# Optimization experiments

Hardware: AMD Instinct MI355X
Metric: run time of the kernel (lower is better)

Reference implementation:

```python
import jax, jax.numpy as jnp
import numpy as np

N, E, DIN, HID, HEADS = 50000, 400000, 256, 64, 4
EPS_BN = 1e-5

def setup_inputs() -> dict:
    key = jax.random.key(0)
    ks = jax.random.split(key, 12)
    inp = {}
    inp['x'] = jax.random.normal(ks[0], (N, DIN), dtype=jnp.float32)
    inp['edge_index'] = jax.random.randint(ks[1], (2, E), 0, N, dtype=jnp.int64)
    s = 1.0 / np.sqrt(DIN)
    inp['W1'] = jax.random.uniform(ks[2], (DIN, HEADS * HID), jnp.float32, -s, s)
    inp['a_src1'] = jax.random.normal(ks[3], (HEADS, HID), dtype=jnp.float32) * 0.1
    inp['a_dst1'] = jax.random.normal(ks[4], (HEADS, HID), dtype=jnp.float32) * 0.1
    inp['b1'] = jnp.zeros((HEADS * HID,), jnp.float32)
    inp['bn1_w'] = jnp.ones((HEADS * HID,), jnp.float32)
    inp['bn1_b'] = jnp.zeros((HEADS * HID,), jnp.float32)
    inp['bn1_m'] = jnp.zeros((HEADS * HID,), jnp.float32)
    inp['bn1_v'] = jnp.ones((HEADS * HID,), jnp.float32)
    s2 = 1.0 / np.sqrt(HEADS * HID)
    inp['W2'] = jax.random.uniform(ks[5], (HEADS * HID, HID), jnp.float32, -s2, s2)
    inp['a_src2'] = jax.random.normal(ks[6], (1, HID), dtype=jnp.float32) * 0.1
    inp['a_dst2'] = jax.random.normal(ks[7], (1, HID), dtype=jnp.float32) * 0.1
    inp['b2'] = jnp.zeros((HID,), jnp.float32)
    inp['bn2_w'] = jnp.ones((HID,), jnp.float32)
    inp['bn2_b'] = jnp.zeros((HID,), jnp.float32)
    inp['bn2_m'] = jnp.zeros((HID,), jnp.float32)
    inp['bn2_v'] = jnp.ones((HID,), jnp.float32)
    sr = 1.0 / np.sqrt(HID)
    inp['Wr'] = jax.random.uniform(ks[8], (HID, 1), jnp.float32, -sr, sr)
    inp['br'] = jnp.zeros((1,), jnp.float32)
    inp['Wc'] = jax.random.uniform(ks[9], (HID, 1), jnp.float32, -sr, sr)
    inp['bc'] = jnp.zeros((1,), jnp.float32)
    return inp

def gat_layer(x, src, dst, W, a_src, a_dst, bias, concat):
    # x: [N, Fin] -> h: [N, H, D]
    H, D = a_src.shape
    h = (x @ W).reshape(-1, H, D)
    alpha_s = jnp.sum(h * a_src[None], axis=-1)  # [N, H]
    alpha_d = jnp.sum(h * a_dst[None], axis=-1)
    e = jax.nn.leaky_relu(alpha_s[src] + alpha_d[dst], 0.2)  # [Et, H]
    m = jax.ops.segment_max(e, dst, num_segments=N)
    m = jnp.where(jnp.isfinite(m), m, 0.0)
    ex = jnp.exp(e - m[dst])
    denom = jax.ops.segment_sum(ex, dst, num_segments=N)
    alpha = ex / (denom[dst] + 1e-16)  # segment softmax over incoming edges
    msg = h[src] * alpha[:, :, None]  # [Et, H, D]
    out = jax.ops.segment_sum(msg, dst, num_segments=N)  # [N, H, D]
    out = out.reshape(N, H * D) if concat else out.mean(axis=1)
    return out + bias

def batchnorm(x, w, b, mean, var):
    return (x - mean) * jax.lax.rsqrt(var + EPS_BN) * w + b

def reference(x, edge_index, W1, a_src1, a_dst1, b1, bn1_w, bn1_b, bn1_m, bn1_v,
              W2, a_src2, a_dst2, b2, bn2_w, bn2_b, bn2_m, bn2_v, Wr, br, Wc, bc):
    # add self loops (PyG GATConv default)
    loops = jnp.arange(N, dtype=edge_index.dtype)
    src = jnp.concatenate([edge_index[0], loops])
    dst = jnp.concatenate([edge_index[1], loops])
    h = gat_layer(x, src, dst, W1, a_src1, a_dst1, b1, concat=True)
    h = jax.nn.elu(batchnorm(h, bn1_w, bn1_b, bn1_m, bn1_v))
    h = gat_layer(h, src, dst, W2, a_src2, a_dst2, b2, concat=False)
    h = jax.nn.elu(batchnorm(h, bn2_w, bn2_b, bn2_m, bn2_v))
    reg = h @ Wr + br
    clf = jax.nn.sigmoid(h @ Wc + bc)
    return reg, clf
```

## Files before the change

kernel.cpp:

```cpp
#include <hip/hip_runtime.h>
#include <math.h>


typedef unsigned short ushort_t;
typedef unsigned char uchar_t;
typedef __attribute__((ext_vector_type(8))) unsigned short ushort8;
typedef __attribute__((ext_vector_type(4))) unsigned short ushort4v;
typedef __attribute__((ext_vector_type(8))) short short8;
typedef __attribute__((ext_vector_type(4))) float f32x4;
typedef __attribute__((ext_vector_type(2))) float f32x2;

#define EPS_BN 1e-5f

__device__ __forceinline__ ushort_t f2bf(float f) {
  unsigned u = __float_as_uint(f);
  unsigned r = u + 0x7fffu + ((u >> 16) & 1u);
  return (ushort_t)(r >> 16);
}
__device__ __forceinline__ float bf2f(ushort_t h) {
  return __uint_as_float((unsigned)h << 16);
}
__device__ __forceinline__ uchar_t f2fp8(float f) {
  return (uchar_t)(__builtin_amdgcn_cvt_pk_fp8_f32(f, f, 0, false) & 0xff);
}
__device__ __forceinline__ void fp8x8_to_f32(uint2 q, float* f) {
  f32x2 a = __builtin_amdgcn_cvt_pk_f32_fp8(q.x, false);
  f32x2 b = __builtin_amdgcn_cvt_pk_f32_fp8(q.x, true);
  f32x2 c = __builtin_amdgcn_cvt_pk_f32_fp8(q.y, false);
  f32x2 d = __builtin_amdgcn_cvt_pk_f32_fp8(q.y, true);
  f[0] = a.x; f[1] = a.y; f[2] = b.x; f[3] = b.y;
  f[4] = c.x; f[5] = c.y; f[6] = d.x; f[7] = d.y;
}
__device__ __forceinline__ float leaky02(float x) { return x >= 0.f ? x : 0.2f * x; }
__device__ __forceinline__ float elu_fast(float x) {
  return x > 0.f ? x : __expf(x) - 1.f;
}
__device__ __forceinline__ float wave_sum(float v) {
#pragma unroll
  for (int o = 1; o < 64; o <<= 1) v += __shfl_xor(v, o, 64);
  return v;
}
__device__ __forceinline__ int wave_incl_scan(int v, int lane) {
#pragma unroll
  for (int off = 1; off < 64; off <<= 1) {
    int t = __shfl_up(v, off, 64);
    if (lane >= off) v += t;
  }
  return v;
}

__device__ __forceinline__ void gld_lds16(const ushort_t* g, ushort_t* l) {
  __builtin_amdgcn_global_load_lds(
      (const __attribute__((address_space(1))) unsigned int*)g,
      (__attribute__((address_space(3))) unsigned int*)l, 16, 0, 0);
}

__global__ void hist_kernel(const int* __restrict__ dst, int* __restrict__ counts, int E) {
  int e = blockIdx.x * blockDim.x + threadIdx.x;
  if (e < E) atomicAdd(&counts[dst[e]], 1);
}

__global__ __launch_bounds__(256) void scan_chunks_kernel(
    const int* __restrict__ counts, int* __restrict__ offsets, int* __restrict__ partials,
    int N, int E, int* __restrict__ csr_src,
    const float* __restrict__ W1, const float* __restrict__ W2,
    ushort_t* __restrict__ W1t, ushort_t* __restrict__ W2t,
    const float* __restrict__ b1, const float* __restrict__ bn1w,
    const float* __restrict__ bn1b, const float* __restrict__ bn1m,
    const float* __restrict__ bn1v,
    const float* __restrict__ b2, const float* __restrict__ bn2w,
    const float* __restrict__ bn2b, const float* __restrict__ bn2m,
    const float* __restrict__ bn2v,
    float* __restrict__ S1, float* __restrict__ T1,
    float* __restrict__ S2, float* __restrict__ T2) {
  __shared__ int ws[4];
  const int tid = threadIdx.x, lane = tid & 63, wv = tid >> 6;
  const int i = blockIdx.x * 256 + tid;
  const int gsz = gridDim.x * 256;
  int v = (i < N) ? counts[i] : 0;
  int incl = wave_incl_scan(v, lane);
  if (lane == 63) ws[wv] = incl;
  __syncthreads();
  int wbase = 0;
  for (int k = 0; k < wv; ++k) wbase += ws[k];
  if (i < N) offsets[i] = wbase + incl - v;
  if (tid == 255) partials[blockIdx.x] = wbase + incl;

  for (int j = i; j < 256 * 256; j += gsz) {
    int k = j >> 8, n2 = j & 255;
    W1t[n2 * 256 + k] = f2bf(W1[j]);
  }
  for (int j = i; j < 256 * 64; j += gsz) {
    int k = j >> 6, n2 = j & 63;
    W2t[n2 * 256 + k] = f2bf(W2[j]);
  }
  if (i < 256) {
    float s = bn1w[i] * rsqrtf(bn1v[i] + EPS_BN);
    S1[i] = s;
    T1[i] = (b1[i] - bn1m[i]) * s + bn1b[i];
  } else if (i < 320) {
    int j = i - 256;
    float s = bn2w[j] * rsqrtf(bn2v[j] + EPS_BN);
    S2[j] = s;
    T2[j] = (b2[j] - bn2m[j]) * s + bn2b[j];
  } else if (i < 384) {
    csr_src[E + i - 320] = 0;
  }
}

__global__ __launch_bounds__(256) void scatter_kernel(
    const int* __restrict__ src, const int* __restrict__ dst,
    const int* __restrict__ offsets, const int* __restrict__ partials,
    int* __restrict__ cursor, int* __restrict__ csr_src,
    int* __restrict__ offs2, int E, int N, int nb) {
  __shared__ int pp[256];
  __shared__ int ws[4];
  __shared__ int tot;
  const int tid = threadIdx.x, lane = tid & 63, wv = tid >> 6;
  int v = (tid < nb) ? partials[tid] : 0;
  int incl = wave_incl_scan(v, lane);
  if (lane == 63) ws[wv] = incl;
  __syncthreads();
  int wbase = 0;
  for (int k = 0; k < wv; ++k) wbase += ws[k];
  pp[tid] = wbase + incl - v;
  if (tid == 255) tot = wbase + incl;
  __syncthreads();

  int idx = blockIdx.x * 256 + tid;
  if (idx < E) {
    int d = dst[idx];
    int p = atomicAdd(&cursor[d], 1);
    csr_src[offsets[d] + pp[d >> 8] + p] = src[idx];
  }
  if (idx <= N) {
    offs2[idx] = (idx < N) ? offsets[idx] + pp[idx >> 8] : tot;
  }
}

template <int WM, bool CASTA, int SWZ, int OUT8>
__global__ __launch_bounds__(WM * 64) void mfma_gemm_fused(
    const void* __restrict__ Ain, const ushort_t* __restrict__ Bt,
    void* __restrict__ Cout, const float* __restrict__ avs, const float* __restrict__ avd,
    float* __restrict__ as_out, float* __restrict__ ad_out, int M, int Nt, int K, int H) {
  constexpr int BM = WM * 32;
  constexpr int NB = 4 / WM;
  __shared__ ushort_t As[BM * 32];
  __shared__ ushort_t Bs[64 * 32];
  const int t = threadIdx.x;
  const int w = t >> 6, l = t & 63;
  int m0, n0;
  if (SWZ) {
    const int Mtile = (M + BM - 1) / BM;
    const int full = (Mtile & ~7) * 4;
    int id = blockIdx.x, r, c;
    if (id < full) {
      int grp = id >> 5, wd = id & 31;
      r = grp * 8 + (wd & 7);
      c = wd >> 3;
    } else {
      int tl = id - full;
      r = (Mtile & ~7) + (tl >> 2);
      c = tl & 3;
    }
    m0 = r * BM;
    n0 = c * 64;
  } else {
    m0 = blockIdx.y * BM;
    n0 = blockIdx.x * 64;
  }
  const int head = n0 >> 6;

  f32x4 zero4 = {0.f, 0.f, 0.f, 0.f};
  f32x4 acc[2][4];
#pragma unroll
  for (int i = 0; i < 2; ++i)
#pragma unroll
    for (int j = 0; j < 4; ++j) acc[i][j] = zero4;

  const int scol = (l & 3) * 8;
  const ushort_t* Bgb[NB];
  ushort_t* Bsl[NB];
#pragma unroll
  for (int b = 0; b < NB; ++b) {
    int r = (b * WM + w) * 16 + (l >> 2);
    Bgb[b] = Bt + (size_t)(n0 + r) * K + scol;
    Bsl[b] = &Bs[(b * WM + w) * 512];
  }
  const ushort_t* Aga[2];
  ushort_t* Asl[2];
  const float* Axg = nullptr;
  ushort_t* AsWc = nullptr;
  if (CASTA) {
    int ar = t >> 1, ac = (t & 1) * 16;
    Axg = (const float*)Ain + (size_t)min(m0 + ar, M - 1) * K + ac;
    AsWc = &As[ar * 32 + ac];
  } else {
#pragma unroll
    for (int a = 0; a < 2; ++a) {
      int r = (a * WM + w) * 16 + (l >> 2);
      int gr = min(m0 + r, M - 1);
      Aga[a] = (const ushort_t*)Ain + (size_t)gr * K + scol;
      Asl[a] = &As[(a * WM + w) * 512];
    }
  }

  for (int k0 = 0; k0 < K; k0 += 32) {
    if (CASTA) {
      float4 f0 = *(const float4*)(Axg + k0);
      float4 f1 = *(const float4*)(Axg + k0 + 4);
      float4 f2 = *(const float4*)(Axg + k0 + 8);
      float4 f3 = *(const float4*)(Axg + k0 + 12);
      __syncthreads();
#pragma unroll
      for (int b = 0; b < NB; ++b) gld_lds16(Bgb[b] + k0, Bsl[b]);
      ushort8 u0, u1;
      u0[0] = f2bf(f0.x); u0[1] = f2bf(f0.y); u0[2] = f2bf(f0.z); u0[3] = f2bf(f0.w);
      u0[4] = f2bf(f1.x); u0[5] = f2bf(f1.y); u0[6] = f2bf(f1.z); u0[7] = f2bf(f1.w);
      u1[0] = f2bf(f2.x); u1[1] = f2bf(f2.y); u1[2] = f2bf(f2.z); u1[3] = f2bf(f2.w);
      u1[4] = f2bf(f3.x); u1[5] = f2bf(f3.y); u1[6] = f2bf(f3.z); u1[7] = f2bf(f3.w);
      *(ushort8*)AsWc = u0;
      *(ushort8*)(AsWc + 8) = u1;
      __syncthreads();
    } else {
      __syncthreads();
#pragma unroll
      for (int a = 0; a < 2; ++a) gld_lds16(Aga[a] + k0, Asl[a]);
#pragma unroll
      for (int b = 0; b < NB; ++b) gld_lds16(Bgb[b] + k0, Bsl[b]);
      __syncthreads();
    }
    const int kq = (l >> 4) * 8;
    short8 af[2], bfr[4];
#pragma unroll
    for (int i = 0; i < 2; ++i)
      af[i] = *(const short8*)&As[(w * 32 + i * 16 + (l & 15)) * 32 + kq];
#pragma unroll
    for (int j = 0; j < 4; ++j)
      bfr[j] = *(const short8*)&Bs[(j * 16 + (l & 15)) * 32 + kq];
#pragma unroll
    for (int i = 0; i < 2; ++i)
#pragma unroll
      for (int j = 0; j < 4; ++j)
        acc[i][j] = __builtin_amdgcn_mfma_f32_16x16x32_bf16(af[i], bfr[j], acc[i][j], 0, 0, 0);
  }

  const int rbase = m0 + w * 32 + (l >> 4) * 4;
  const int cbase = n0 + (l & 15);
#pragma unroll
  for (int i = 0; i < 2; ++i)
#pragma unroll
    for (int j = 0; j < 4; ++j)
#pragma unroll
      for (int r = 0; r < 4; ++r) {
        int row = rbase + i * 16 + r;
        if (row < M) {
          if (OUT8)
            ((uchar_t*)Cout)[(size_t)row * Nt + cbase + j * 16] = f2fp8(acc[i][j][r]);
          else
            ((ushort_t*)Cout)[(size_t)row * Nt + cbase + j * 16] = f2bf(acc[i][j][r]);
        }
      }

  float asw[4], adw[4];
#pragma unroll
  for (int j = 0; j < 4; ++j) {
    asw[j] = avs[head * 64 + (l & 15) + j * 16];
    adw[j] = avd[head * 64 + (l & 15) + j * 16];
  }
#pragma unroll
  for (int i = 0; i < 2; ++i)
#pragma unroll
    for (int r = 0; r < 4; ++r) {
      float s_ = acc[i][0][r] * asw[0] + acc[i][1][r] * asw[1] +
                 acc[i][2][r] * asw[2] + acc[i][3][r] * asw[3];
      float d_ = acc[i][0][r] * adw[0] + acc[i][1][r] * adw[1] +
                 acc[i][2][r] * adw[2] + acc[i][3][r] * adw[3];
#pragma unroll
      for (int o = 1; o < 16; o <<= 1) {
        s_ += __shfl_xor(s_, o, 64);
        d_ += __shfl_xor(d_, o, 64);
      }
      if ((l & 15) == 0) {
        int row = rbase + i * 16 + r;
        if (row < M) {
          as_out[(size_t)row * H + head] = s_;
          ad_out[(size_t)row * H + head] = d_;
        }
      }
    }
}

__global__ __launch_bounds__(256) void agg1_kernel(
    const uchar_t* __restrict__ h1, const int* __restrict__ offsets,
    const int* __restrict__ csr, const float* __restrict__ as1,
    const float* __restrict__ ad1,
    const float* __restrict__ S1, const float* __restrict__ T1,
    ushort_t* __restrict__ out, int N) {
  __shared__ float ldsW[4][64][4];
  __shared__ int ldsS[4][64];
  const int wv = threadIdx.x >> 6;
  int n = blockIdx.x * 4 + wv;
  int l = threadIdx.x & 63;
  if (n >= N) return;
  const int g = l >> 5, ll = l & 31, hh = ll >> 3;
  int off = offsets[n], deg = offsets[n + 1] - off;
  const int* csrp = csr + off;
  const size_t hoff = (size_t)ll * 8;
  float4 adn = *(const float4*)&ad1[n * 4];

  float acc[8] = {0, 0, 0, 0, 0, 0, 0, 0};
  float ds[4] = {0, 0, 0, 0};

  for (int base = 0; base < deg; base += 64) {
    int cnt = min(64, deg - base);
    int s = 0;
    float4 w4 = make_float4(0.f, 0.f, 0.f, 0.f);
    if (l < cnt) {
      s = csrp[base + l];
      float4 a4 = *(const float4*)&as1[s * 4];
      w4.x = __expf(leaky02(a4.x + adn.x));
      w4.y = __expf(leaky02(a4.y + adn.y));
      w4.z = __expf(leaky02(a4.z + adn.z));
      w4.w = __expf(leaky02(a4.w + adn.w));
    }
    ldsS[wv][l] = s;
    *(float4*)&ldsW[wv][l][0] = w4;
    ds[0] += w4.x; ds[1] += w4.y; ds[2] += w4.z; ds[3] += w4.w;
    for (int j = 0; j < cnt; j += 8) {
      int e0 = j + g, e1 = j + 2 + g, e2 = j + 4 + g, e3 = j + 6 + g;
      int s0 = ldsS[wv][e0], s1 = ldsS[wv][e1], s2 = ldsS[wv][e2], s3 = ldsS[wv][e3];
      float w0 = ldsW[wv][e0][hh], w1 = ldsW[wv][e1][hh];
      float w2 = ldsW[wv][e2][hh], w3 = ldsW[wv][e3][hh];
      uint2 q0 = *(const uint2*)&h1[(size_t)s0 * 256 + hoff];
      uint2 q1 = *(const uint2*)&h1[(size_t)s1 * 256 + hoff];
      uint2 q2 = *(const uint2*)&h1[(size_t)s2 * 256 + hoff];
      uint2 q3 = *(const uint2*)&h1[(size_t)s3 * 256 + hoff];
      float f0[8], f1[8], f2[8], f3[8];
      fp8x8_to_f32(q0, f0);
      fp8x8_to_f32(q1, f1);
      fp8x8_to_f32(q2, f2);
      fp8x8_to_f32(q3, f3);
#pragma unroll
      for (int k = 0; k < 8; ++k) acc[k] = fmaf(w0, f0[k], acc[k]);
#pragma unroll
      for (int k = 0; k < 8; ++k) acc[k] = fmaf(w1, f1[k], acc[k]);
#pragma unroll
      for (int k = 0; k < 8; ++k) acc[k] = fmaf(w2, f2[k], acc[k]);
#pragma unroll
      for (int k = 0; k < 8; ++k) acc[k] = fmaf(w3, f3[k], acc[k]);
    }
  }
#pragma unroll
  for (int k = 0; k < 8; ++k) acc[k] += __shfl_xor(acc[k], 32, 64);
  float den[4];
#pragma unroll
  for (int h = 0; h < 4; ++h) den[h] = wave_sum(ds[h]);

  float4 asn = *(const float4*)&as1[n * 4];
  float wsf[4];
  wsf[0] = __expf(leaky02(asn.x + adn.x));
  wsf[1] = __expf(leaky02(asn.y + adn.y));
  wsf[2] = __expf(leaky02(asn.z + adn.z));
  wsf[3] = __expf(leaky02(asn.w + adn.w));
  uint2 qn = *(const uint2*)&h1[(size_t)n * 256 + hoff];
  float fn[8];
  fp8x8_to_f32(qn, fn);
  float wsh = wsf[hh];
#pragma unroll
  for (int k = 0; k < 8; ++k) acc[k] = fmaf(wsh, fn[k], acc[k]);
  float inv = 1.f / (den[hh] + wsh + 1e-16f);

  int c0 = ll * 8 + g * 4;
  float4 Sv = *(const float4*)&S1[c0];
  float4 Tv = *(const float4*)&T1[c0];
  float Sf[4] = {Sv.x, Sv.y, Sv.z, Sv.w};
  float Tf[4] = {Tv.x, Tv.y, Tv.z, Tv.w};
  ushort4v o4;
#pragma unroll
  for (int q = 0; q < 4; ++q) {
    float o = fmaf(acc[g * 4 + q], inv * Sf[q], Tf[q]);
    o4[q] = f2bf(elu_fast(o));
  }
  *(ushort4v*)&out[(size_t)n * 256 + c0] = o4;
}

__global__ __launch_bounds__(256) void agg2_kernel(
    const ushort_t* __restrict__ h2, const int* __restrict__ offsets,
    const int* __restrict__ csr, const float* __restrict__ as2,
    const float* __restrict__ ad2,
    const float* __restrict__ S2, const float* __restrict__ T2,
    const float* __restrict__ Wr, const float* __restrict__ br,
    const float* __restrict__ Wc, const float* __restrict__ bc,
    float* __restrict__ out_reg, float* __restrict__ out_clf, int N) {
  __shared__ float ldsW[4][64];
  __shared__ int ldsS[4][64];
  const int wv = threadIdx.x >> 6;
  int n = blockIdx.x * 4 + wv;
  int l = threadIdx.x & 63;
  if (n >= N) return;
  const int g = l >> 4, ll = l & 15;
  int off = offsets[n], deg = offsets[n + 1] - off;
  const int* csrp = csr + off;
  const size_t hoff = (size_t)ll * 4;
  float adn = ad2[n];

  float acc[4] = {0, 0, 0, 0};
  float ds = 0.f;

  for (int base = 0; base < deg; base += 64) {
    int cnt = min(64, deg - base);
    int s = 0;
    float wv_ = 0.f;
    if (l < cnt) {
      s = csrp[base + l];
      wv_ = __expf(leaky02(as2[s] + adn));
    }
    ldsS[wv][l] = s;
    ldsW[wv][l] = wv_;
    ds += wv_;
    for (int j = 0; j < cnt; j += 16) {
      int e0 = j + g, e1 = j + 4 + g, e2 = j + 8 + g, e3 = j + 12 + g;
      int s0 = ldsS[wv][e0], s1 = ldsS[wv][e1], s2 = ldsS[wv][e2], s3 = ldsS[wv][e3];
      float w0 = ldsW[wv][e0], w1 = ldsW[wv][e1], w2 = ldsW[wv][e2], w3 = ldsW[wv][e3];
      ushort4v r0 = *(const ushort4v*)&h2[(size_t)s0 * 64 + hoff];
      ushort4v r1 = *(const ushort4v*)&h2[(size_t)s1 * 64 + hoff];
      ushort4v r2 = *(const ushort4v*)&h2[(size_t)s2 * 64 + hoff];
      ushort4v r3 = *(const ushort4v*)&h2[(size_t)s3 * 64 + hoff];
#pragma unroll
      for (int k = 0; k < 4; ++k) acc[k] = fmaf(w0, bf2f(r0[k]), acc[k]);
#pragma unroll
      for (int k = 0; k < 4; ++k) acc[k] = fmaf(w1, bf2f(r1[k]), acc[k]);
#pragma unroll
      for (int k = 0; k < 4; ++k) acc[k] = fmaf(w2, bf2f(r2[k]), acc[k]);
#pragma unroll
      for (int k = 0; k < 4; ++k) acc[k] = fmaf(w3, bf2f(r3[k]), acc[k]);
    }
  }
#pragma unroll
  for (int k = 0; k < 4; ++k) {
    acc[k] += __shfl_xor(acc[k], 16, 64);
    acc[k] += __shfl_xor(acc[k], 32, 64);
  }
  float den = wave_sum(ds);
  float ws = __expf(leaky02(as2[n] + adn));
  ushort4v hn = *(const ushort4v*)&h2[(size_t)n * 64 + hoff];
#pragma unroll
  for (int k = 0; k < 4; ++k) acc[k] = fmaf(ws, bf2f(hn[k]), acc[k]);
  float inv = 1.f / (den + ws + 1e-16f);

  int c0 = ll * 4;
  float4 Sv = *(const float4*)&S2[c0];
  float4 Tv = *(const float4*)&T2[c0];
  float4 wr = *(const float4*)&Wr[c0];
  float4 wc = *(const float4*)&Wc[c0];
  float Sf[4] = {Sv.x, Sv.y, Sv.z, Sv.w};
  float Tf[4] = {Tv.x, Tv.y, Tv.z, Tv.w};
  float wrf[4] = {wr.x, wr.y, wr.z, wr.w};
  float wcf[4] = {wc.x, wc.y, wc.z, wc.w};
  float rs = 0.f, cs = 0.f;
#pragma unroll
  for (int q = 0; q < 4; ++q) {
    float o = fmaf(acc[q], inv * Sf[q], Tf[q]);
    o = elu_fast(o);
    rs = fmaf(o, wrf[q], rs);
    cs = fmaf(o, wcf[q], cs);
  }
#pragma unroll
  for (int o = 1; o < 16; o <<= 1) {
    rs += __shfl_xor(rs, o, 64);
    cs += __shfl_xor(cs, o, 64);
  }
  if (l == 0) {
    out_reg[n] = rs + br[0];
    float z = cs + bc[0];
    out_clf[n] = 1.f / (1.f + __expf(-z));
  }
}

extern "C" void kernel_launch(void* const* d_in, const int* in_sizes, int n_in,
                              void* d_out, int out_size, void* d_ws, size_t ws_size,
                              hipStream_t stream) {
  const float* x      = (const float*)d_in[0];
  const int*   ei     = (const int*)d_in[1];
  const float* W1     = (const float*)d_in[2];
  const float* a_src1 = (const float*)d_in[3];
  const float* a_dst1 = (const float*)d_in[4];
  const float* b1     = (const float*)d_in[5];
  const float* bn1w   = (const float*)d_in[6];
  const float* bn1b   = (const float*)d_in[7];
  const float* bn1m   = (const float*)d_in[8];
  const float* bn1v   = (const float*)d_in[9];
  const float* W2     = (const float*)d_in[10];
  const float* a_src2 = (const float*)d_in[11];
  const float* a_dst2 = (const float*)d_in[12];
  const float* b2     = (const float*)d_in[13];
  const float* bn2w   = (const float*)d_in[14];
  const float* bn2b   = (const float*)d_in[15];
  const float* bn2m   = (const float*)d_in[16];
  const float* bn2v   = (const float*)d_in[17];
  const float* Wr     = (const float*)d_in[18];
  const float* br     = (const float*)d_in[19];
  const float* Wc     = (const float*)d_in[20];
  const float* bc     = (const float*)d_in[21];

  const int N = in_sizes[0] / 256;
  const int E = in_sizes[1] / 2;
  const int* srcv = ei;
  const int* dstv = ei + E;

  char* w = (char*)d_ws;
  auto alloc = [&](size_t bytes) {
    char* p = w;
    w += (bytes + 255) & ~(size_t)255;
    return p;
  };
  const int nb = (N + 255) / 256;
  const size_t nbytes_rounded = ((size_t)N * 4 + 255) & ~(size_t)255;
  int* counts    = (int*)alloc((size_t)N * 4);
  int* cursor    = (int*)alloc((size_t)N * 4);
  int* offsets   = (int*)alloc((size_t)N * 4);
  int* offs2     = (int*)alloc((size_t)(N + 1) * 4);
  int* partials  = (int*)alloc((size_t)nb * 4);
  int* csr_src   = (int*)alloc((size_t)(E + 64) * 4);
  float* as1     = (float*)alloc((size_t)N * 4 * 4);
  float* ad1     = (float*)alloc((size_t)N * 4 * 4);
  float* as2     = (float*)alloc((size_t)N * 4);
  float* ad2     = (float*)alloc((size_t)N * 4);
  float* S1      = (float*)alloc(256 * 4);
  float* T1      = (float*)alloc(256 * 4);
  float* S2      = (float*)alloc(64 * 4);
  float* T2      = (float*)alloc(64 * 4);
  ushort_t* W1t  = (ushort_t*)alloc((size_t)256 * 256 * 2);
  ushort_t* W2t  = (ushort_t*)alloc((size_t)64 * 256 * 2);
  uchar_t* h1b   = (uchar_t*)alloc((size_t)N * 256);
  ushort_t* h1a  = (ushort_t*)alloc((size_t)N * 256 * 2);
  ushort_t* h2b  = (ushort_t*)alloc((size_t)N * 64 * 2);

  float* out_reg = (float*)d_out;

  hipMemsetAsync(counts, 0, nbytes_rounded * 2, stream);
  hist_kernel<<<(E + 255) / 256, 256, 0, stream>>>(dstv, counts, E);
  scan_chunks_kernel<<<nb, 256, 0, stream>>>(counts, offsets, partials, N, E, csr_src,
                                             W1, W2, W1t, W2t,
                                             b1, bn1w, bn1b, bn1m, bn1v,
                                             b2, bn2w, bn2b, bn2m, bn2v,
                                             S1, T1, S2, T2);
  {
    int items = max(E, N + 1);
    scatter_kernel<<<(items + 255) / 256, 256, 0, stream>>>(srcv, dstv, offsets, partials,
                                                            cursor, csr_src, offs2, E, N, nb);
  }

  const int nwb = (N + 3) / 4;

  const int mtiles = (N + 127) / 128;
  mfma_gemm_fused<4, true, 1, 1><<<mtiles * 4, 256, 0, stream>>>(
      x, W1t, h1b, a_src1, a_dst1, as1, ad1, N, 256, 256, 4);
  agg1_kernel<<<nwb, 256, 0, stream>>>(h1b, offs2, csr_src, as1, ad1, S1, T1, h1a, N);

  dim3 g2(1, (N + 63) / 64);
  mfma_gemm_fused<2, false, 0, 0><<<g2, 128, 0, stream>>>(h1a, W2t, h2b, a_src2, a_dst2,
                                                          as2, ad2, N, 64, 256, 1);
  agg2_kernel<<<nwb, 256, 0, stream>>>(h2b, offs2, csr_src, as2, ad2, S2, T2,
                                       Wr, br, Wc, bc, out_reg, out_reg + N, N);
}
```

Baseline: 267.3 us.

## Remap agg1 lanes so the whole wave gathers one full edge row

```diff
diff --git a/kernel.cpp b/kernel.cpp
--- a/kernel.cpp
+++ b/kernel.cpp
@@ -298,19 +298,19 @@
     const float* __restrict__ S1, const float* __restrict__ T1,
     ushort_t* __restrict__ out, int N) {
   __shared__ float ldsW[4][64][4];
-  __shared__ int ldsS[4][64];
   const int wv = threadIdx.x >> 6;
   int n = blockIdx.x * 4 + wv;
   int l = threadIdx.x & 63;
   if (n >= N) return;
-  const int g = l >> 5, ll = l & 31, hh = ll >> 3;
+  const int hh = l >> 4;
   int off = offsets[n], deg = offsets[n + 1] - off;
   const int* csrp = csr + off;
-  const size_t hoff = (size_t)ll * 8;
+  const unsigned fb = (unsigned)l << 2;
   float4 adn = *(const float4*)&ad1[n * 4];
-
-  float acc[8] = {0, 0, 0, 0, 0, 0, 0, 0};
-  float ds[4] = {0, 0, 0, 0};
+  float ad_h = (hh & 2) ? ((hh & 1) ? adn.w : adn.z) : ((hh & 1) ? adn.y : adn.x);
+
+  f32x2 acc0 = {0.f, 0.f}, acc1 = {0.f, 0.f};
+  float den = 0.f;
 
   for (int base = 0; base < deg; base += 64) {
     int cnt = min(64, deg - base);
@@ -324,64 +324,49 @@
       w4.z = __expf(leaky02(a4.z + adn.z));
       w4.w = __expf(leaky02(a4.w + adn.w));
     }
-    ldsS[wv][l] = s;
     *(float4*)&ldsW[wv][l][0] = w4;
-    ds[0] += w4.x; ds[1] += w4.y; ds[2] += w4.z; ds[3] += w4.w;
     for (int j = 0; j < cnt; j += 8) {
-      int e0 = j + g, e1 = j + 2 + g, e2 = j + 4 + g, e3 = j + 6 + g;
-      int s0 = ldsS[wv][e0], s1 = ldsS[wv][e1], s2 = ldsS[wv][e2], s3 = ldsS[wv][e3];
-      float w0 = ldsW[wv][e0][hh], w1 = ldsW[wv][e1][hh];
-      float w2 = ldsW[wv][e2][hh], w3 = ldsW[wv][e3][hh];
-      uint2 q0 = *(const uint2*)&h1[(size_t)s0 * 256 + hoff];
-      uint2 q1 = *(const uint2*)&h1[(size_t)s1 * 256 + hoff];
-      uint2 q2 = *(const uint2*)&h1[(size_t)s2 * 256 + hoff];
-      uint2 q3 = *(const uint2*)&h1[(size_t)s3 * 256 + hoff];
-      float f0[8], f1[8], f2[8], f3[8];
-      fp8x8_to_f32(q0, f0);
-      fp8x8_to_f32(q1, f1);
-      fp8x8_to_f32(q2, f2);
-      fp8x8_to_f32(q3, f3);
-#pragma unroll
-      for (int k = 0; k < 8; ++k) acc[k] = fmaf(w0, f0[k], acc[k]);
-#pragma unroll
-      for (int k = 0; k < 8; ++k) acc[k] = fmaf(w1, f1[k], acc[k]);
-#pragma unroll
-      for (int k = 0; k < 8; ++k) acc[k] = fmaf(w2, f2[k], acc[k]);
-#pragma unroll
-      for (int k = 0; k < 8; ++k) acc[k] = fmaf(w3, f3[k], acc[k]);
-    }
-  }
-#pragma unroll
-  for (int k = 0; k < 8; ++k) acc[k] += __shfl_xor(acc[k], 32, 64);
-  float den[4];
-#pragma unroll
-  for (int h = 0; h < 4; ++h) den[h] = wave_sum(ds[h]);
+#pragma unroll
+      for (int i = 0; i < 8; ++i) {
+        int e = j + i;
+        unsigned se = (unsigned)__builtin_amdgcn_readlane(s, e);
+        float we = ldsW[wv][e][hh];
+        unsigned q = *(const unsigned*)(h1 + (size_t)((se << 8) + fb));
+        f32x2 lo = __builtin_amdgcn_cvt_pk_f32_fp8(q, false);
+        f32x2 hi = __builtin_amdgcn_cvt_pk_f32_fp8(q, true);
+        f32x2 w2 = {we, we};
+        acc0 = lo * w2 + acc0;
+        acc1 = hi * w2 + acc1;
+        den += we;
+      }
+    }
+  }
 
   float4 asn = *(const float4*)&as1[n * 4];
-  float wsf[4];
-  wsf[0] = __expf(leaky02(asn.x + adn.x));
-  wsf[1] = __expf(leaky02(asn.y + adn.y));
-  wsf[2] = __expf(leaky02(asn.z + adn.z));
-  wsf[3] = __expf(leaky02(asn.w + adn.w));
-  uint2 qn = *(const uint2*)&h1[(size_t)n * 256 + hoff];
-  float fn[8];
-  fp8x8_to_f32(qn, fn);
-  float wsh = wsf[hh];
-#pragma unroll
-  for (int k = 0; k < 8; ++k) acc[k] = fmaf(wsh, fn[k], acc[k]);
-  float inv = 1.f / (den[hh] + wsh + 1e-16f);
-
-  int c0 = ll * 8 + g * 4;
+  float as_h = (hh & 2) ? ((hh & 1) ? asn.w : asn.z) : ((hh & 1) ? asn.y : asn.x);
+  float ws = __expf(leaky02(as_h + ad_h));
+  {
+    unsigned q = *(const unsigned*)(h1 + (size_t)(((unsigned)n << 8) + fb));
+    f32x2 lo = __builtin_amdgcn_cvt_pk_f32_fp8(q, false);
+    f32x2 hi = __builtin_amdgcn_cvt_pk_f32_fp8(q, true);
+    f32x2 w2 = {ws, ws};
+    acc0 = lo * w2 + acc0;
+    acc1 = hi * w2 + acc1;
+  }
+  float inv = 1.f / (den + ws + 1e-16f);
+
+  const int c0 = l * 4;
   float4 Sv = *(const float4*)&S1[c0];
   float4 Tv = *(const float4*)&T1[c0];
-  float Sf[4] = {Sv.x, Sv.y, Sv.z, Sv.w};
-  float Tf[4] = {Tv.x, Tv.y, Tv.z, Tv.w};
+  float o0 = fmaf(acc0.x, inv * Sv.x, Tv.x);
+  float o1 = fmaf(acc0.y, inv * Sv.y, Tv.y);
+  float o2 = fmaf(acc1.x, inv * Sv.z, Tv.z);
+  float o3 = fmaf(acc1.y, inv * Sv.w, Tv.w);
   ushort4v o4;
-#pragma unroll
-  for (int q = 0; q < 4; ++q) {
-    float o = fmaf(acc[g * 4 + q], inv * Sf[q], Tf[q]);
-    o4[q] = f2bf(elu_fast(o));
-  }
+  o4[0] = f2bf(elu_fast(o0));
+  o4[1] = f2bf(elu_fast(o1));
+  o4[2] = f2bf(elu_fast(o2));
+  o4[3] = f2bf(elu_fast(o3));
   *(ushort4v*)&out[(size_t)n * 256 + c0] = o4;
 }
 
```

Result: faster. 261.5 us (-2.2%).
